# Kernel tuning notes

Measured on AMD Instinct MI355X. Metric: run time of the kernel, lower is better.

The kernel has to match this reference:

```python
import jax, jax.numpy as jnp
import numpy as np

N = 50000
E = 1_600_000
IN_C = 128
HID = 128
HEADS = 4
F_OUT = HID // HEADS  # 32
NEG_SLOPE = 0.2


def _glorot(key, shape):
    fan_in, fan_out = shape[0], shape[-1]
    lim = jnp.sqrt(6.0 / (fan_in + fan_out)).astype(jnp.float32)
    return jax.random.uniform(key, shape, jnp.float32, -lim, lim)


def setup_inputs() -> dict:
    key = jax.random.key(0)
    ks = jax.random.split(key, 12)
    x = jax.random.normal(ks[0], (N, IN_C), jnp.float32)
    edge_index = jax.random.randint(ks[1], (2, E), 0, N, jnp.int32)
    # layer 0 params
    W0 = _glorot(ks[2], (IN_C, HEADS * F_OUT))
    att_src0 = _glorot(ks[3], (HEADS, F_OUT))
    att_dst0 = _glorot(ks[4], (HEADS, F_OUT))
    b0 = jnp.zeros((HEADS * F_OUT,), jnp.float32)
    # layer 1 params
    W1 = _glorot(ks[5], (HID, HEADS * F_OUT))
    att_src1 = _glorot(ks[6], (HEADS, F_OUT))
    att_dst1 = _glorot(ks[7], (HEADS, F_OUT))
    b1 = jnp.zeros((HEADS * F_OUT,), jnp.float32)
    return {"x": x, "edge_index": edge_index,
            "W0": W0, "att_src0": att_src0, "att_dst0": att_dst0, "b0": b0,
            "W1": W1, "att_src1": att_src1, "att_dst1": att_dst1, "b1": b1}


def gat_conv(x, src, dst, W, att_src, att_dst, b):
    n = x.shape[0]
    h = (x @ W).reshape(n, HEADS, F_OUT)              # [N,H,F]
    a_s = jnp.einsum('nhf,hf->nh', h, att_src)        # [N,H]
    a_d = jnp.einsum('nhf,hf->nh', h, att_dst)        # [N,H]
    e = jax.nn.leaky_relu(a_s[src] + a_d[dst], NEG_SLOPE)   # [E,H]
    # segment softmax over destination-node neighborhoods
    e_max = jax.ops.segment_max(e, dst, num_segments=n)     # [N,H]
    e_exp = jnp.exp(e - e_max[dst])                          # [E,H]
    denom = jax.ops.segment_sum(e_exp, dst, num_segments=n)  # [N,H]
    denom = jnp.where(denom > 0, denom, 1.0)
    alpha = e_exp / denom[dst]                               # [E,H]
    msg = alpha[:, :, None] * h[src]                         # [E,H,F]
    out = jax.ops.segment_sum(msg, dst, num_segments=n)      # [N,H,F]
    return out.reshape(n, HEADS * F_OUT) + b


def reference(x, edge_index, W0, att_src0, att_dst0, b0, W1, att_src1, att_dst1, b1):
    src, dst = edge_index[0], edge_index[1]
    h = gat_conv(x, src, dst, W0, att_src0, att_dst0, b0)
    h = jax.nn.relu(h)  # dropout p=0.0 / eval mode -> identity
    out = gat_conv(h, src, dst, W1, att_src1, att_dst1, b1)
    return out
```

## Files before the change

### kernel.cpp

```cpp
#include <hip/hip_runtime.h>
#include <hip/hip_fp16.h>

#define N_NODES 50000
#define N_EDGES 1600000
#define NB 196
#define NBLK 256
#define CHUNK (N_EDGES / NBLK)
#define SCAN_N (NB * NBLK)

typedef _Float16 half8_t __attribute__((ext_vector_type(8)));
typedef float floatx4 __attribute__((ext_vector_type(4)));

__global__ __launch_bounds__(256) void gemm_mfma(const float* __restrict__ Xf,
                                                 const __half* __restrict__ Xh,
                                                 int in_half,
                                                 const float* __restrict__ W,
                                                 const float* __restrict__ att_s,
                                                 const float* __restrict__ att_d,
                                                 __half* __restrict__ H16,
                                                 float* __restrict__ as_out,
                                                 float* __restrict__ ad_out, int nrows) {
    __shared__ __align__(16) char lds[49152];
    char* Alds = lds;
    char* Wlds = lds + 16384;
    int t = threadIdx.x;
    int lane = t & 63, wv_ = t >> 6;
    for (int p = 0; p < 16; ++p) {
        int flat = p * 256 + t;
        int k = flat >> 5;
        int n0 = (flat & 31) * 4;
        float4 wv = reinterpret_cast<const float4*>(W)[flat];
        const float* wf = reinterpret_cast<const float*>(&wv);
        #pragma unroll
        for (int i = 0; i < 4; ++i) {
            int n = n0 + i;
            int byte = (n * 256 + k * 2) ^ ((n & 7) << 4);
            *reinterpret_cast<__half*>(Wlds + byte) = __float2half(wf[i]);
        }
    }
    int col16 = lane & 15;
    float Asv[8], Adv[8];
    #pragma unroll
    for (int nt = 0; nt < 8; ++nt) {
        Asv[nt] = att_s[nt * 16 + col16];
        Adv[nt] = att_d[nt * 16 + col16];
    }
    int ksub = (lane >> 4) * 16;
    int rloc = wv_ * 16 + col16;
    int ntiles = (nrows + 63) / 64;
    for (int tile = blockIdx.x; tile < ntiles; tile += gridDim.x) {
        int row0 = tile * 64;
        __syncthreads();
        for (int p = 0; p < 8; ++p) {
            int r = p * 8 + (t >> 5);
            int f4 = t & 31;
            int rr = row0 + r;
            uint2 hv = make_uint2(0, 0);
            if (rr < nrows) {
                if (in_half) {
                    hv = *reinterpret_cast<const uint2*>(Xh + (size_t)rr * 128 + f4 * 4);
                } else {
                    float4 xv = reinterpret_cast<const float4*>(Xf)[(size_t)rr * 32 + f4];
                    __half2* hp = reinterpret_cast<__half2*>(&hv);
                    hp[0] = __floats2half2_rn(xv.x, xv.y);
                    hp[1] = __floats2half2_rn(xv.z, xv.w);
                }
            }
            int byte = (r * 256 + f4 * 8) ^ ((r & 7) << 4);
            *reinterpret_cast<uint2*>(Alds + byte) = hv;
        }
        __syncthreads();
        half8_t afr[4];
        #pragma unroll
        for (int kb = 0; kb < 4; ++kb) {
            int byte = (rloc * 256 + kb * 64 + ksub) ^ ((rloc & 7) << 4);
            afr[kb] = *reinterpret_cast<half8_t*>(Alds + byte);
        }
        floatx4 acc[8];
        #pragma unroll
        for (int nt = 0; nt < 8; ++nt) {
            int n = nt * 16 + col16;
            floatx4 a = {0.f, 0.f, 0.f, 0.f};
            #pragma unroll
            for (int kb = 0; kb < 4; ++kb) {
                int byte = (n * 256 + kb * 64 + ksub) ^ ((n & 7) << 4);
                half8_t bfr = *reinterpret_cast<half8_t*>(Wlds + byte);
                a = __builtin_amdgcn_mfma_f32_16x16x32_f16(afr[kb], bfr, a, 0, 0, 0);
            }
            acc[nt] = a;
        }
        float ps[4][4], pd[4][4];
        #pragma unroll
        for (int reg = 0; reg < 4; ++reg)
            #pragma unroll
            for (int h = 0; h < 4; ++h) {
                ps[reg][h] = acc[2*h][reg] * Asv[2*h] + acc[2*h+1][reg] * Asv[2*h+1];
                pd[reg][h] = acc[2*h][reg] * Adv[2*h] + acc[2*h+1][reg] * Adv[2*h+1];
            }
        #pragma unroll
        for (int m = 1; m <= 8; m <<= 1)
            #pragma unroll
            for (int reg = 0; reg < 4; ++reg)
                #pragma unroll
                for (int h = 0; h < 4; ++h) {
                    ps[reg][h] += __shfl_xor(ps[reg][h], m);
                    pd[reg][h] += __shfl_xor(pd[reg][h], m);
                }
        int rbase = row0 + wv_ * 16 + (lane >> 4) * 4;
        #pragma unroll
        for (int reg = 0; reg < 4; ++reg) {
            int grow = rbase + reg;
            if (grow < nrows) {
                #pragma unroll
                for (int nt = 0; nt < 8; ++nt)
                    H16[(size_t)grow * 128 + nt * 16 + col16] = __float2half(acc[nt][reg]);
                if (col16 == 0) {
                    *reinterpret_cast<float4*>(as_out + (size_t)grow * 4) =
                        make_float4(ps[reg][0], ps[reg][1], ps[reg][2], ps[reg][3]);
                    *reinterpret_cast<float4*>(ad_out + (size_t)grow * 4) =
                        make_float4(pd[reg][0], pd[reg][1], pd[reg][2], pd[reg][3]);
                }
            }
        }
    }
}

__global__ __launch_bounds__(1024) void bucket_hist(const int* __restrict__ dst,
                                                    int* __restrict__ counts) {
    __shared__ int hist[NB];
    int t = threadIdx.x, b = blockIdx.x;
    if (t < NB) hist[t] = 0;
    __syncthreads();
    int s = b * CHUNK;
    for (int i = t; i < CHUNK; i += 1024)
        atomicAdd(&hist[dst[s + i] >> 8], 1);
    __syncthreads();
    if (t < NB) counts[t * NBLK + b] = hist[t];
}

__global__ __launch_bounds__(1024) void scan_all(const int* __restrict__ counts,
                                                 int* __restrict__ start) {
    __shared__ int sh[1024];
    int t = threadIdx.x;
    int base = t * 49;
    int sum = 0;
    for (int i = 0; i < 49; ++i) sum += counts[base + i];
    sh[t] = sum;
    __syncthreads();
    for (int off = 1; off < 1024; off <<= 1) {
        int v = (t >= off) ? sh[t - off] : 0;
        __syncthreads();
        sh[t] += v;
        __syncthreads();
    }
    int run = sh[t] - sum;
    for (int i = 0; i < 49; ++i) {
        int c = counts[base + i];
        start[base + i] = run;
        run += c;
    }
}

__global__ __launch_bounds__(1024) void bucket_scatter(const int* __restrict__ src,
                                                       const int* __restrict__ dst,
                                                       const int* __restrict__ start,
                                                       int* __restrict__ bucketed) {
    __shared__ int cur[NB];
    int t = threadIdx.x, b = blockIdx.x;
    if (t < NB) cur[t] = start[t * NBLK + b];
    __syncthreads();
    int s = b * CHUNK;
    for (int i = t; i < CHUNK; i += 1024) {
        int d = dst[s + i];
        int p = atomicAdd(&cur[d >> 8], 1);
        bucketed[p] = (src[s + i] << 8) | (d & 255);
    }
}

__global__ __launch_bounds__(1024) void bucket_sort(const int* __restrict__ bucketed,
                                                    const int* __restrict__ start,
                                                    int* __restrict__ sorted_packed,
                                                    int* __restrict__ off) {
    __shared__ int cnt[256], scn[256], cur[256];
    int t = threadIdx.x, k = blockIdx.x;
    int base = start[k * NBLK];
    int end = (k + 1 < NB) ? start[(k + 1) * NBLK] : N_EDGES;
    int m = end - base;
    if (t < 256) cnt[t] = 0;
    __syncthreads();
    for (int i = t; i < m; i += 1024)
        atomicAdd(&cnt[bucketed[base + i] & 255], 1);
    __syncthreads();
    if (t < 256) scn[t] = cnt[t];
    __syncthreads();
    for (int o = 1; o < 256; o <<= 1) {
        int v = (t < 256 && t >= o) ? scn[t - o] : 0;
        __syncthreads();
        if (t < 256) scn[t] += v;
        __syncthreads();
    }
    if (t < 256) {
        int excl = scn[t] - cnt[t];
        cur[t] = base + excl;
        int node = k * 256 + t;
        if (node <= N_NODES) off[node] = base + excl;
    }
    __syncthreads();
    for (int i = t; i < m; i += 1024) {
        int rec = bucketed[base + i];
        int p = atomicAdd(&cur[rec & 255], 1);
        sorted_packed[p] = rec;
    }
}

__global__ __launch_bounds__(256) void gat_aggregate_f(const __half* __restrict__ H16,
                                                       const int* __restrict__ off,
                                                       const int* __restrict__ packed,
                                                       const float* __restrict__ asb,
                                                       const float* __restrict__ adb,
                                                       const float* __restrict__ bias,
                                                       float* __restrict__ OUTF,
                                                       __half* __restrict__ OUTH,
                                                       int n, int mode ) {
    int wid = (blockIdx.x * 256 + threadIdx.x) >> 6;
    int lane = threadIdx.x & 63;
    if (wid >= n) return;
    int s = off[wid], e = off[wid + 1];
    int q = lane >> 4;
    int sub = lane & 15;
    int head = sub >> 2;
    int sub16 = sub * 16;
    float adv = adb[(size_t)wid * 4 + head];
    const char* Hc = reinterpret_cast<const char*>(H16);
    const char* Ac = reinterpret_cast<const char*>(asb);
    float acc[8] = {0, 0, 0, 0, 0, 0, 0, 0};
    float den = 0.f;
    for (int i = s; i < e; i += 8) {
        int ia = i + q, ib = ia + 4;
        bool va = ia < e, vb = ib < e;
        int ja = va ? ia : s, jb = vb ? ib : s;
        int ra = packed[ja], rb = packed[jb];
        int ba = ra & 0xFFFFFF00, bb = rb & 0xFFFFFF00;
        float sa = *reinterpret_cast<const float*>(Ac + (ba >> 4) + head * 4);
        float sb = *reinterpret_cast<const float*>(Ac + (bb >> 4) + head * 4);
        uint4 ha = *reinterpret_cast<const uint4*>(Hc + ba + sub16);
        uint4 hb = *reinterpret_cast<const uint4*>(Hc + bb + sub16);
        float ea = sa + adv; ea = fmaxf(ea, 0.2f * ea);
        float eb = sb + adv; eb = fmaxf(eb, 0.2f * eb);
        float wa = va ? __expf(ea) : 0.f;
        float wb = vb ? __expf(eb) : 0.f;
        const __half2* pa = reinterpret_cast<const __half2*>(&ha);
        const __half2* pb = reinterpret_cast<const __half2*>(&hb);
        #pragma unroll
        for (int j = 0; j < 4; ++j) {
            float2 fa = __half22float2(pa[j]);
            float2 fb = __half22float2(pb[j]);
            acc[2*j]   += wa * fa.x + wb * fb.x;
            acc[2*j+1] += wa * fa.y + wb * fb.y;
        }
        den += wa + wb;
    }
    #pragma unroll
    for (int j = 0; j < 8; ++j) acc[j] += __shfl_xor(acc[j], 16);
    den += __shfl_xor(den, 16);
    #pragma unroll
    for (int j = 0; j < 8; ++j) acc[j] += __shfl_xor(acc[j], 32);
    den += __shfl_xor(den, 32);
    if (q == 0) {
        float inv = den > 0.f ? 1.f / den : 0.f;
        float4 b0 = *reinterpret_cast<const float4*>(bias + sub * 8);
        float4 b1 = *reinterpret_cast<const float4*>(bias + sub * 8 + 4);
        float o[8];
        o[0] = acc[0]*inv + b0.x; o[1] = acc[1]*inv + b0.y;
        o[2] = acc[2]*inv + b0.z; o[3] = acc[3]*inv + b0.w;
        o[4] = acc[4]*inv + b1.x; o[5] = acc[5]*inv + b1.y;
        o[6] = acc[6]*inv + b1.z; o[7] = acc[7]*inv + b1.w;
        if (mode) {
            uint4 u;
            __half2* up = reinterpret_cast<__half2*>(&u);
            #pragma unroll
            for (int j = 0; j < 4; ++j)
                up[j] = __floats2half2_rn(fmaxf(o[2*j], 0.f), fmaxf(o[2*j+1], 0.f));
            *reinterpret_cast<uint4*>(OUTH + (size_t)wid * 128 + sub * 8) = u;
        } else {
            *reinterpret_cast<float4*>(OUTF + (size_t)wid * 128 + sub * 8) =
                make_float4(o[0], o[1], o[2], o[3]);
            *reinterpret_cast<float4*>(OUTF + (size_t)wid * 128 + sub * 8 + 4) =
                make_float4(o[4], o[5], o[6], o[7]);
        }
    }
}

extern "C" void kernel_launch(void* const* d_in, const int* in_sizes, int n_in,
                              void* d_out, int out_size, void* d_ws, size_t ws_size,
                              hipStream_t stream) {
    const float* x        = (const float*)d_in[0];
    const int*   edge     = (const int*)d_in[1];
    const float* W0       = (const float*)d_in[2];
    const float* att_src0 = (const float*)d_in[3];
    const float* att_dst0 = (const float*)d_in[4];
    const float* b0       = (const float*)d_in[5];
    const float* W1       = (const float*)d_in[6];
    const float* att_src1 = (const float*)d_in[7];
    const float* att_dst1 = (const float*)d_in[8];
    const float* b1       = (const float*)d_in[9];
    const int* src = edge;
    const int* dst = edge + N_EDGES;
    float* out = (float*)d_out;

    char* ws = (char*)d_ws;
    size_t o = 0;
    auto alloc = [&](size_t bytes) { char* p = ws + o; o += (bytes + 255) & ~(size_t)255; return p; };
    __half* H16   = (__half*)alloc((size_t)N_NODES * 128 * 2);
    float* asb    = (float*)alloc((size_t)N_NODES * 4 * 4);
    float* adb    = (float*)alloc((size_t)N_NODES * 4 * 4);
    int*   off    = (int*)alloc((size_t)(N_NODES + 1) * 4);
    int*   sorted = (int*)alloc((size_t)N_EDGES * 4);
    size_t mark = o;
    int*   counts = (int*)alloc((size_t)SCAN_N * 4);
    int*   start  = (int*)alloc((size_t)SCAN_N * 4);
    int*   bucketed = (int*)alloc((size_t)N_EDGES * 4);
    __half* h1_16 = (__half*)(ws + mark);

    bucket_hist<<<NBLK, 1024, 0, stream>>>(dst, counts);
    scan_all<<<1, 1024, 0, stream>>>(counts, start);
    bucket_scatter<<<NBLK, 1024, 0, stream>>>(src, dst, start, bucketed);
    bucket_sort<<<NB, 1024, 0, stream>>>(bucketed, start, sorted, off);

    int agg_blocks = (N_NODES + 3) / 4;

    gemm_mfma<<<256, 256, 0, stream>>>(x, (const __half*)nullptr, 0, W0, att_src0, att_dst0,
                                       H16, asb, adb, N_NODES);
    gat_aggregate_f<<<agg_blocks, 256, 0, stream>>>(H16, off, sorted, asb, adb, b0,
                                                    (float*)nullptr, h1_16, N_NODES, 1);

    gemm_mfma<<<256, 256, 0, stream>>>((const float*)nullptr, h1_16, 1, W1, att_src1, att_dst1,
                                       H16, asb, adb, N_NODES);
    gat_aggregate_f<<<agg_blocks, 256, 0, stream>>>(H16, off, sorted, asb, adb, b1,
                                                    out, (__half*)nullptr, N_NODES, 0);
}
```

Baseline: 222.4 us.

## Fuse destination histogram into first GEMM and software-pipeline aggregation with fdot2

Removes the separate bucket_hist launch by appending histogram blocks to the first GEMM grid, so the histogram runs concurrently with the layer-0 projection. The aggregation kernel now prefetches the next edge's packed index and attention score one iteration ahead, which hides the dependent load latency. It also packs two edge weights into a half2 and uses fdot2 so each pair of FMAs is done in one instruction. Using fp16 weights in fdot2 reduces the precision of the attention weights, and the histogram blocks compete with GEMM blocks for LDS and compute units.

```diff
diff --git a/kernel.cpp b/kernel.cpp
--- a/kernel.cpp
+++ b/kernel.cpp
@@ -7,9 +7,20 @@
 #define NBLK 256
 #define CHUNK (N_EDGES / NBLK)
 #define SCAN_N (NB * NBLK)
+#define GEMM_BLOCKS 256
 
 typedef _Float16 half8_t __attribute__((ext_vector_type(8)));
+typedef _Float16 half2_t __attribute__((ext_vector_type(2)));
 typedef float floatx4 __attribute__((ext_vector_type(4)));
+
+#if defined(__has_builtin)
+#  if __has_builtin(__builtin_amdgcn_fdot2)
+#    define HAS_FDOT2 1
+#  endif
+#endif
+#ifndef HAS_FDOT2
+#  define HAS_FDOT2 0
+#endif
 
 __global__ __launch_bounds__(256) void gemm_mfma(const float* __restrict__ Xf,
                                                  const __half* __restrict__ Xh,
@@ -19,11 +30,25 @@
                                                  const float* __restrict__ att_d,
                                                  __half* __restrict__ H16,
                                                  float* __restrict__ as_out,
-                                                 float* __restrict__ ad_out, int nrows) {
+                                                 float* __restrict__ ad_out, int nrows,
+                                                 const int* __restrict__ hist_dst,
+                                                 int* __restrict__ hist_counts) {
     __shared__ __align__(16) char lds[49152];
+    int t = threadIdx.x;
+    if (hist_counts != nullptr && blockIdx.x >= GEMM_BLOCKS) {
+        int* hist = reinterpret_cast<int*>(lds);
+        int b = blockIdx.x - GEMM_BLOCKS;
+        for (int i = t; i < NB; i += 256) hist[i] = 0;
+        __syncthreads();
+        int s = b * CHUNK;
+        for (int i = t; i < CHUNK; i += 256)
+            atomicAdd(&hist[hist_dst[s + i] >> 8], 1);
+        __syncthreads();
+        for (int i = t; i < NB; i += 256) hist_counts[i * NBLK + b] = hist[i];
+        return;
+    }
     char* Alds = lds;
     char* Wlds = lds + 16384;
-    int t = threadIdx.x;
     int lane = t & 63, wv_ = t >> 6;
     for (int p = 0; p < 16; ++p) {
         int flat = p * 256 + t;
@@ -48,7 +73,7 @@
     int ksub = (lane >> 4) * 16;
     int rloc = wv_ * 16 + col16;
     int ntiles = (nrows + 63) / 64;
-    for (int tile = blockIdx.x; tile < ntiles; tile += gridDim.x) {
+    for (int tile = blockIdx.x; tile < ntiles; tile += GEMM_BLOCKS) {
         int row0 = tile * 64;
         __syncthreads();
         for (int p = 0; p < 8; ++p) {
@@ -125,19 +150,6 @@
     }
 }
 
-__global__ __launch_bounds__(1024) void bucket_hist(const int* __restrict__ dst,
-                                                    int* __restrict__ counts) {
-    __shared__ int hist[NB];
-    int t = threadIdx.x, b = blockIdx.x;
-    if (t < NB) hist[t] = 0;
-    __syncthreads();
-    int s = b * CHUNK;
-    for (int i = t; i < CHUNK; i += 1024)
-        atomicAdd(&hist[dst[s + i] >> 8], 1);
-    __syncthreads();
-    if (t < NB) counts[t * NBLK + b] = hist[t];
-}
-
 __global__ __launch_bounds__(1024) void scan_all(const int* __restrict__ counts,
                                                  int* __restrict__ start) {
     __shared__ int sh[1024];
@@ -213,52 +225,73 @@
     }
 }
 
-__global__ __launch_bounds__(256) void gat_aggregate_f(const __half* __restrict__ H16,
-                                                       const int* __restrict__ off,
-                                                       const int* __restrict__ packed,
-                                                       const float* __restrict__ asb,
-                                                       const float* __restrict__ adb,
-                                                       const float* __restrict__ bias,
-                                                       float* __restrict__ OUTF,
-                                                       __half* __restrict__ OUTH,
-                                                       int n, int mode ) {
+__global__ __launch_bounds__(256) void gat_aggregate_v2(const __half* __restrict__ H16,
+                                                        const int* __restrict__ off,
+                                                        const int* __restrict__ packed,
+                                                        const float* __restrict__ asb,
+                                                        const float* __restrict__ adb,
+                                                        const float* __restrict__ bias,
+                                                        float* __restrict__ OUTF,
+                                                        __half* __restrict__ OUTH,
+                                                        int n, int mode) {
     int wid = (blockIdx.x * 256 + threadIdx.x) >> 6;
     int lane = threadIdx.x & 63;
     if (wid >= n) return;
     int s = off[wid], e = off[wid + 1];
     int q = lane >> 4;
     int sub = lane & 15;
-    int head = sub >> 2;
+    int head4 = (sub >> 2) * 4;
     int sub16 = sub * 16;
-    float adv = adb[(size_t)wid * 4 + head];
+    float adv = adb[(size_t)wid * 4 + (sub >> 2)];
     const char* Hc = reinterpret_cast<const char*>(H16);
     const char* Ac = reinterpret_cast<const char*>(asb);
     float acc[8] = {0, 0, 0, 0, 0, 0, 0, 0};
     float den = 0.f;
-    for (int i = s; i < e; i += 8) {
-        int ia = i + q, ib = ia + 4;
-        bool va = ia < e, vb = ib < e;
-        int ja = va ? ia : s, jb = vb ? ib : s;
-        int ra = packed[ja], rb = packed[jb];
-        int ba = ra & 0xFFFFFF00, bb = rb & 0xFFFFFF00;
-        float sa = *reinterpret_cast<const float*>(Ac + (ba >> 4) + head * 4);
-        float sb = *reinterpret_cast<const float*>(Ac + (bb >> 4) + head * 4);
-        uint4 ha = *reinterpret_cast<const uint4*>(Hc + ba + sub16);
-        uint4 hb = *reinterpret_cast<const uint4*>(Hc + bb + sub16);
-        float ea = sa + adv; ea = fmaxf(ea, 0.2f * ea);
-        float eb = sb + adv; eb = fmaxf(eb, 0.2f * eb);
-        float wa = va ? __expf(ea) : 0.f;
-        float wb = vb ? __expf(eb) : 0.f;
-        const __half2* pa = reinterpret_cast<const __half2*>(&ha);
-        const __half2* pb = reinterpret_cast<const __half2*>(&hb);
-        #pragma unroll
-        for (int j = 0; j < 4; ++j) {
-            float2 fa = __half22float2(pa[j]);
-            float2 fb = __half22float2(pb[j]);
-            acc[2*j]   += wa * fa.x + wb * fb.x;
-            acc[2*j+1] += wa * fa.y + wb * fb.y;
-        }
-        den += wa + wb;
+    if (s < e) {
+        int ia = s + q, ib = ia + 4;
+        int ja = ia < e ? ia : s, jb = ib < e ? ib : s;
+        int ra = packed[ja] & 0xFFFFFF00;
+        int rb = packed[jb] & 0xFFFFFF00;
+        float sa = *reinterpret_cast<const float*>(Ac + (ra >> 4) + head4);
+        float sb = *reinterpret_cast<const float*>(Ac + (rb >> 4) + head4);
+        for (int i = s; i < e; i += 8) {
+            uint4 ha = *reinterpret_cast<const uint4*>(Hc + ra + sub16);
+            uint4 hb = *reinterpret_cast<const uint4*>(Hc + rb + sub16);
+            bool va = (i + q) < e, vb = (i + q + 4) < e;
+            float ea = sa + adv; ea = fmaxf(ea, 0.2f * ea);
+            float eb = sb + adv; eb = fmaxf(eb, 0.2f * eb);
+            float wa = va ? __expf(ea) : 0.f;
+            float wb = vb ? __expf(eb) : 0.f;
+            int ia2 = i + 8 + q, ib2 = ia2 + 4;
+            int ja2 = ia2 < e ? ia2 : s, jb2 = ib2 < e ? ib2 : s;
+            ra = packed[ja2] & 0xFFFFFF00;
+            rb = packed[jb2] & 0xFFFFFF00;
+            sa = *reinterpret_cast<const float*>(Ac + (ra >> 4) + head4);
+            sb = *reinterpret_cast<const float*>(Ac + (rb >> 4) + head4);
+            den += wa + wb;
+#if HAS_FDOT2
+            half2_t w01 = __builtin_bit_cast(half2_t, __builtin_amdgcn_cvt_pkrtz(wa, wb));
+            const uint* hau = reinterpret_cast<const uint*>(&ha);
+            const uint* hbu = reinterpret_cast<const uint*>(&hb);
+            #pragma unroll
+            for (int j = 0; j < 4; ++j) {
+                uint p0 = __builtin_amdgcn_perm(hbu[j], hau[j], 0x05040100u);
+                uint p1 = __builtin_amdgcn_perm(hbu[j], hau[j], 0x07060302u);
+                acc[2*j]   = __builtin_amdgcn_fdot2(__builtin_bit_cast(half2_t, p0), w01, acc[2*j],   false);
+                acc[2*j+1] = __builtin_amdgcn_fdot2(__builtin_bit_cast(half2_t, p1), w01, acc[2*j+1], false);
+            }
+#else
+            const __half2* pa = reinterpret_cast<const __half2*>(&ha);
+            const __half2* pb = reinterpret_cast<const __half2*>(&hb);
+            #pragma unroll
+            for (int j = 0; j < 4; ++j) {
+                float2 fa = __half22float2(pa[j]);
+                float2 fb = __half22float2(pb[j]);
+                acc[2*j]   += wa * fa.x + wb * fb.x;
+                acc[2*j+1] += wa * fa.y + wb * fb.y;
+            }
+#endif
+        }
     }
     #pragma unroll
     for (int j = 0; j < 8; ++j) acc[j] += __shfl_xor(acc[j], 16);
@@ -322,20 +355,22 @@
     int*   bucketed = (int*)alloc((size_t)N_EDGES * 4);
     __half* h1_16 = (__half*)(ws + mark);
 
-    bucket_hist<<<NBLK, 1024, 0, stream>>>(dst, counts);
+    int agg_blocks = N_NODES / 4;
+
+    gemm_mfma<<<GEMM_BLOCKS + NBLK, 256, 0, stream>>>(x, (const __half*)nullptr, 0,
+                                                      W0, att_src0, att_dst0,
+                                                      H16, asb, adb, N_NODES, dst, counts);
     scan_all<<<1, 1024, 0, stream>>>(counts, start);
     bucket_scatter<<<NBLK, 1024, 0, stream>>>(src, dst, start, bucketed);
     bucket_sort<<<NB, 1024, 0, stream>>>(bucketed, start, sorted, off);
 
-    int agg_blocks = (N_NODES + 3) / 4;
-
-    gemm_mfma<<<256, 256, 0, stream>>>(x, (const __half*)nullptr, 0, W0, att_src0, att_dst0,
-                                       H16, asb, adb, N_NODES);
-    gat_aggregate_f<<<agg_blocks, 256, 0, stream>>>(H16, off, sorted, asb, adb, b0,
-                                                    (float*)nullptr, h1_16, N_NODES, 1);
-
-    gemm_mfma<<<256, 256, 0, stream>>>((const float*)nullptr, h1_16, 1, W1, att_src1, att_dst1,
-                                       H16, asb, adb, N_NODES);
-    gat_aggregate_f<<<agg_blocks, 256, 0, stream>>>(H16, off, sorted, asb, adb, b1,
-                                                    out, (__half*)nullptr, N_NODES, 0);
-}
+    gat_aggregate_v2<<<agg_blocks, 256, 0, stream>>>(H16, off, sorted, asb, adb, b0,
+                                                     (float*)nullptr, h1_16, N_NODES, 1);
+
+    gemm_mfma<<<GEMM_BLOCKS, 256, 0, stream>>>((const float*)nullptr, h1_16, 1,
+                                               W1, att_src1, att_dst1,
+                                               H16, asb, adb, N_NODES,
+                                               (const int*)nullptr, (int*)nullptr);
+    gat_aggregate_v2<<<agg_blocks, 256, 0, stream>>>(H16, off, sorted, asb, adb, b1,
+                                                     out, (__half*)nullptr, N_NODES, 0);
+}
```

New measurement: 212.9 us. 1.04x faster.
